# Kernel tuning notes

Hardware: AMD Instinct MI355X
Metric: run time of the kernel (lower is better)

The kernel has to match this reference:

```python
import collections
import functools
import itertools
import math
import jax
import jax.numpy as jnp
import numpy as np

# Weight space: RNN-like {W_ih:(784,512), W_hh:(512,512), b:(512,)}, channels last.
N0, N1, C_IN, C_OUT = 784, 512, 16, 16
PERM_SPEC = [[0, 1], [1, 1], [1]]  # perm-group label per dim of each leaf
N_TERMS = [11, 25, 9]  # equivariant basis terms per output leaf (Bell-number products)


def diagonal_slice(X, matching_dims):
    out = jnp.diagonal(X, axis1=matching_dims[0], axis2=matching_dims[1])
    for dim in matching_dims[2:]:
        out = jnp.diagonal(out, axis1=dim, axis2=-1)
    return out


def find_missing_indices(lstA, lstB):
    setB = set(lstB)
    return [i for i, el in enumerate(lstA) if el not in setB]


def get_repeated_idcs(lst):
    index_map = {}
    for index, item in enumerate(lst):
        index_map.setdefault(item, []).append(index)
    return [idcs for idcs in index_map.values() if len(idcs) > 1]


def match_dim_order(X, X_idcs, out_idcs):
    X_idcs_copy = X_idcs[:]
    perm = []
    for idx in out_idcs:
        if idx in X_idcs_copy:
            i = X_idcs_copy.index(idx)
            perm.append(i)
            X_idcs_copy[i] = None
    X = jnp.transpose(X, perm)
    return X, [X_idcs[i] for i in perm]


def remove_idcs(lst, idcs):
    return [l for i, l in enumerate(lst) if i not in idcs]


def move_dims_to_end(X, dims):
    new_in_order = remove_idcs(list(range(X.ndim)), dims) + dims
    return jnp.transpose(X, new_in_order)


def generate_partitions(items):
    if len(items) == 1:
        yield [items]
        return
    first = items[0]
    for subpart in generate_partitions(items[1:]):
        for n, subset in enumerate(subpart):
            yield subpart[:n] + [[first] + subset] + subpart[n + 1:]
        yield [[first]] + subpart


def valid_partitions(indices, perms):
    groups = collections.defaultdict(list)
    for index, perm in zip(indices, perms):
        groups[perm].append(index)
    parts_per_group = [list(generate_partitions(g)) for g in groups.values()]
    for p in itertools.product(*parts_per_group):
        yield [s for s in itertools.chain(*p)]


def gen_terms(out_spec, in_spec, out_shape, inp):
    """Basis terms of an equivariant linear map from in_spec to out_spec."""
    terms = []
    k1, k2 = len(out_spec), len(in_spec)
    for partition in valid_partitions(list(range(k1 + k2)), list(out_spec) + list(in_spec)):
        indices = [-1] * (k1 + k2)
        for subset_idx, subset in enumerate(partition):
            for dim in subset:
                indices[dim] = subset_idx
        out_indices, in_indices = indices[:k1], indices[k1:]
        term = inp
        # Collapse repeated input indices via diagonals.
        while (rep_idcs := get_repeated_idcs(in_indices)):
            term = diagonal_slice(term, rep_idcs[0])
            idx = in_indices[rep_idcs[0][0]]
            in_indices = remove_idcs(in_indices, rep_idcs[0])
            in_indices.append(idx)
        # Mean-reduce input dims that do not appear in the output.
        agg_idcs = find_missing_indices(in_indices, out_indices)
        term = jnp.mean(term, axis=agg_idcs)
        in_indices = remove_idcs(in_indices, agg_idcs)
        # Scatter onto diagonals for repeated output indices.
        for diag_set in get_repeated_idcs(out_indices):
            dim_size, out_idx = out_shape[diag_set[0]], out_indices[diag_set[0]]
            matching_in_dims = [i for i, idx in enumerate(in_indices) if idx == out_idx]
            num_new_dims = len(diag_set) - len(matching_in_dims)
            term = move_dims_to_end(term, matching_in_dims)
            new_term = jnp.zeros(term.shape + (dim_size,) * num_new_dims, dtype=term.dtype)
            diag_slice = (jnp.s_[:],) * (new_term.ndim - len(diag_set)) + (jnp.arange(dim_size),) * len(diag_set)
            if not matching_in_dims:
                term = jnp.expand_dims(term, axis=-1)
            term = new_term.at[diag_slice].add(term)
            in_indices = remove_idcs(in_indices, matching_in_dims)
            in_indices.extend([out_idx] * len(diag_set))
        term, in_indices = match_dim_order(term, in_indices, out_indices)
        term = jnp.expand_dims(term, axis=find_missing_indices(out_indices, in_indices))
        terms.append(term)
    return terms


def setup_inputs() -> dict:
    key = jax.random.key(0)
    ks = jax.random.split(key, 6)
    inp = {
        "w_ih": jax.random.normal(ks[0], (N0, N1, C_IN), jnp.float32),
        "w_hh": jax.random.normal(ks[1], (N1, N1, C_IN), jnp.float32),
        "b": jax.random.normal(ks[2], (N1, C_IN), jnp.float32),
    }
    for i, n in enumerate(N_TERMS):
        scale = math.sqrt(2.0 / (C_IN * n))  # 'he' init, fan_in = c_in * n_terms
        inp[f"theta_{i}"] = scale * jax.random.normal(ks[3 + i], (n, C_IN, C_OUT), jnp.float32)
        inp[f"bias_{i}"] = jnp.zeros((C_OUT,), jnp.float32)
    return inp


def reference(w_ih, w_hh, b, theta_0, theta_1, theta_2, bias_0, bias_1, bias_2):
    flat_params = [w_ih, w_hh, b]
    thetas = [theta_0, theta_1, theta_2]
    biases = [bias_0, bias_1, bias_2]
    outs = []
    for i in range(3):
        terms_i = []
        for j in range(3):
            gen = jax.vmap(
                functools.partial(gen_terms, PERM_SPEC[i], PERM_SPEC[j], flat_params[i].shape),
                in_axes=-1, out_axes=-1)
            terms_i.extend(gen(flat_params[j]))
        out = biases[i]
        for k, term in enumerate(terms_i):
            out = out + term @ thetas[i][k]  # [..., c_in] @ [c_in, c_out]
        outs.append(out)
    return tuple(outs)
```

## Files before the change

kernel.cpp:

```cpp
#include <hip/hip_runtime.h>


#define N0 784
#define N1 512

typedef float v4f __attribute__((ext_vector_type(4)));
typedef float v2f __attribute__((ext_vector_type(2)));

__device__ __forceinline__ float4 f4add(float4 a, float4 b) {
  a.x += b.x; a.y += b.y; a.z += b.z; a.w += b.w; return a;
}
__device__ __forceinline__ void nt_store4(float* p, float4 v) {
  v4f x; x[0] = v.x; x[1] = v.y; x[2] = v.z; x[3] = v.w;
  __builtin_nontemporal_store(x, (v4f*)p);
}
__device__ __forceinline__ void nt_store2(float* p, float x0, float x1) {
  v2f x; x[0] = x0; x[1] = x1;
  __builtin_nontemporal_store(x, (v2f*)p);
}

__global__ __launch_bounds__(256)
void k_stage1(const float* __restrict__ wih, const float* __restrict__ whh,
              float* __restrict__ rm_ih, float* __restrict__ cm_ih,
              float* __restrict__ rm_hh, float* __restrict__ cm_hh,
              float* __restrict__ d_hh) {
  __shared__ float4 red[256];
  int t = threadIdx.x, blk = blockIdx.x;
  float4 acc = make_float4(0.f, 0.f, 0.f, 0.f);
  float scale;
  float* dst;
  if (blk < N0) {
    const float4* row = (const float4*)(wih + (size_t)blk * 8192);
    for (int j = t; j < 2048; j += 256) acc = f4add(acc, row[j]);
    scale = 1.f / 512.f; dst = rm_ih + blk * 16;
  } else if (blk < N0 + N1) {
    int b = blk - N0, q = t & 3, g = t >> 2;
    for (int a = g; a < N0; a += 64)
      acc = f4add(acc, *(const float4*)(wih + (size_t)a * 8192 + b * 16 + q * 4));
    scale = 1.f / 784.f; dst = cm_ih + b * 16;
  } else if (blk < N0 + 2 * N1) {
    int b = blk - N0 - N1;
    const float4* row = (const float4*)(whh + (size_t)b * 8192);
    for (int j = t; j < 2048; j += 256) acc = f4add(acc, row[j]);
    scale = 1.f / 512.f; dst = rm_hh + b * 16;
  } else {
    int b = blk - N0 - 2 * N1, q = t & 3, g = t >> 2;
    for (int a = g; a < N1; a += 64)
      acc = f4add(acc, *(const float4*)(whh + (size_t)a * 8192 + b * 16 + q * 4));
    scale = 1.f / 512.f; dst = cm_hh + b * 16;
    if (t < 4) ((float4*)(d_hh + b * 16))[t] = *(const float4*)(whh + (size_t)b * 8192 + b * 16 + t * 4);
  }
  red[t] = acc; __syncthreads();
  #pragma unroll
  for (int s = 128; s >= 4; s >>= 1) {
    if (t < s) red[t] = f4add(red[t], red[t + s]);
    __syncthreads();
  }
  if (t < 4) {
    float4 m = red[t];
    ((float4*)dst)[t] = make_float4(m.x * scale, m.y * scale, m.z * scale, m.w * scale);
  }
}

__global__ __launch_bounds__(256)
void k_small(const float* __restrict__ rm_ih, const float* __restrict__ d_hh,
             const float* __restrict__ rm_hh, const float* __restrict__ bvec,
             float* __restrict__ gv_g) {
  __shared__ float4 red[256];
  int t = threadIdx.x, q = t & 3, g = t >> 2;
  const float* src; int n; float scale;
  switch (blockIdx.x) {
    case 0: src = rm_ih; n = N0; scale = 1.f / 784.f; break;
    case 1: src = d_hh;  n = N1; scale = 1.f / 512.f; break;
    case 2: src = rm_hh; n = N1; scale = 1.f / 512.f; break;
    default: src = bvec; n = N1; scale = 1.f / 512.f; break;
  }
  float4 acc = make_float4(0.f, 0.f, 0.f, 0.f);
  for (int a = g; a < n; a += 64) acc = f4add(acc, ((const float4*)src)[a * 4 + q]);
  red[t] = acc; __syncthreads();
  #pragma unroll
  for (int s = 128; s >= 4; s >>= 1) {
    if (t < s) red[t] = f4add(red[t], red[t + s]);
    __syncthreads();
  }
  if (t < 4) {
    float4 m = red[t];
    float* dst = gv_g + blockIdx.x * 16 + t * 4;
    dst[0] = m.x * scale; dst[1] = m.y * scale; dst[2] = m.z * scale; dst[3] = m.w * scale;
  }
}

__global__ __launch_bounds__(256)
void k_vec(const float* __restrict__ rm_ih, const float* __restrict__ cm_ih,
           const float* __restrict__ rm_hh, const float* __restrict__ cm_hh,
           const float* __restrict__ d_hh, const float* __restrict__ bvec,
           const float* __restrict__ gv_g,
           const float* __restrict__ th0, const float* __restrict__ bias0,
           const float* __restrict__ th1, const float* __restrict__ bias1,
           const float* __restrict__ th2, const float* __restrict__ bias2,
           float* __restrict__ A0C, float* __restrict__ B0,
           float* __restrict__ A1C, float* __restrict__ B1,
           float* __restrict__ DD1, float* __restrict__ out2) {
  __shared__ float th[11520];
  __shared__ float gvs[64];
  int t = threadIdx.x;
  {
    float4* t4 = (float4*)th;
    const float4* s0 = (const float4*)th0;
    const float4* s1 = (const float4*)th1;
    const float4* s2 = (const float4*)th2;
    for (int j = t; j < 704; j += 256) t4[j] = s0[j];
    for (int j = t; j < 1600; j += 256) t4[704 + j] = s1[j];
    for (int j = t; j < 576; j += 256) t4[2304 + j] = s2[j];
    if (t < 64) gvs[t] = gv_g[t];
  }
  __syncthreads();
  int co = t & 15;
  float c0 = bias0[co], c1 = bias1[co], e1 = 0.f, s2v = bias2[co];
  #pragma unroll
  for (int j = 0; j < 16; j++) {
    int o = j * 16 + co;
    float g0v = gvs[j], dm = gvs[16 + j], gh = gvs[32 + j], mv = gvs[48 + j];
    c0  += g0v * th[768 + o]         + dm * th[1280 + o]        + gh * th[2048 + o]        + mv * th[2560 + o];
    c1  += g0v * th[2816 + 1024 + o] + dm * th[2816 + 2304 + o] + gh * th[2816 + 4864 + o] + mv * th[2816 + 6144 + o];
    e1  += g0v * th[2816 + 512 + o]  + dm * th[2816 + 1792 + o] + gh * th[2816 + 4096 + o] + mv * th[2816 + 5632 + o];
    s2v += g0v * th[9216 + 256 + o]  + dm * th[9216 + 768 + o]  + gh * th[9216 + 1536 + o] + mv * th[9216 + 2048 + o];
  }
  int idx = blockIdx.x * 256 + t;
  int i = idx >> 4;
  float a0 = c0;
  {
    const float4* r4 = (const float4*)(rm_ih + i * 16);
    #pragma unroll
    for (int kq = 0; kq < 4; kq++) {
      float4 r = r4[kq];
      float vr[4] = { r.x, r.y, r.z, r.w };
      #pragma unroll
      for (int e = 0; e < 4; e++) a0 += vr[e] * th[256 + (kq * 4 + e) * 16 + co];
    }
  }
  A0C[idx] = a0;
  if (i < N1) {
    float b0a = 0.f, a1 = c1, b1a = 0.f, dd = e1, o2 = s2v;
    const float4* c4 = (const float4*)(cm_ih + i * 16);
    const float4* d4 = (const float4*)(d_hh + i * 16);
    const float4* r4 = (const float4*)(rm_hh + i * 16);
    const float4* m4 = (const float4*)(cm_hh + i * 16);
    const float4* v4 = (const float4*)(bvec + i * 16);
    #pragma unroll
    for (int kq = 0; kq < 4; kq++) {
      float4 cq = c4[kq], dq = d4[kq], rq = r4[kq], mq = m4[kq], vq = v4[kq];
      float vc[4] = { cq.x, cq.y, cq.z, cq.w };
      float vd[4] = { dq.x, dq.y, dq.z, dq.w };
      float vr[4] = { rq.x, rq.y, rq.z, rq.w };
      float vm[4] = { mq.x, mq.y, mq.z, mq.w };
      float vb[4] = { vq.x, vq.y, vq.z, vq.w };
      #pragma unroll
      for (int e = 0; e < 4; e++) {
        int o = (kq * 4 + e) * 16 + co;
        float cmi = vc[e], d = vd[e], r = vr[e], cm = vm[e], v = vb[e];
        b0a += cmi * th[512 + o]         + d * th[1024 + o]        + r * th[1536 + o]        + cm * th[1792 + o]        + v * th[2304 + o];
        a1  += cmi * th[2816 + 768 + o]  + d * th[2816 + 2048 + o] + r * th[2816 + 4352 + o] + cm * th[2816 + 4608 + o] + v * th[2816 + 5888 + o];
        b1a += cmi * th[2816 + 256 + o]  + d * th[2816 + 1536 + o] + r * th[2816 + 3072 + o] + cm * th[2816 + 3840 + o] + v * th[2816 + 5376 + o];
        dd  += cmi * th[2816 + 0 + o]    + d * th[2816 + 1280 + o] + r * th[2816 + 2560 + o] + cm * th[2816 + 3584 + o] + v * th[2816 + 5120 + o];
        o2  += cmi * th[9216 + 0 + o]    + d * th[9216 + 512 + o]  + r * th[9216 + 1024 + o] + cm * th[9216 + 1280 + o] + v * th[9216 + 1792 + o];
      }
    }
    B0[idx] = b0a; A1C[idx] = a1; B1[idx] = b1a; DD1[idx] = dd; out2[idx] = o2;
  }
}

__global__ __launch_bounds__(256)
void k_out(const float* __restrict__ wih, const float* __restrict__ whh,
           const float* __restrict__ th0, const float* __restrict__ th1,
           const float* __restrict__ A0C, const float* __restrict__ B0,
           const float* __restrict__ A1C, const float* __restrict__ B1,
           const float* __restrict__ DD1,
           float* __restrict__ out0, float* __restrict__ out1) {
  if (blockIdx.x < 1024) {
    int tid = blockIdx.x * 256 + threadIdx.x;
    int q = tid & 3;
    int slot = tid >> 2;
    const int nslots = (1024 * 256) >> 2;
    float4 tq[16];
    #pragma unroll
    for (int k = 0; k < 16; k++) tq[k] = *(const float4*)(th0 + k * 16 + q * 4);
    for (int p = slot; p < N0 * N1; p += nslots) {
      const float4* row = (const float4*)(wih + (size_t)p * 16);
      float4 r0 = row[0], r1 = row[1], r2 = row[2], r3 = row[3];
      int a = p >> 9, bb = p & 511;
      float4 acc = *(const float4*)(A0C + a * 16 + q * 4);
      float4 b4 = *(const float4*)(B0 + bb * 16 + q * 4);
      acc.x += b4.x; acc.y += b4.y; acc.z += b4.z; acc.w += b4.w;
      float wv[16] = { r0.x, r0.y, r0.z, r0.w, r1.x, r1.y, r1.z, r1.w,
                       r2.x, r2.y, r2.z, r2.w, r3.x, r3.y, r3.z, r3.w };
      #pragma unroll
      for (int k = 0; k < 16; k++) {
        acc.x += wv[k] * tq[k].x; acc.y += wv[k] * tq[k].y;
        acc.z += wv[k] * tq[k].z; acc.w += wv[k] * tq[k].w;
      }
      nt_store4(out0 + (size_t)p * 16 + q * 4, acc);
    }
  } else {
    int tid = (blockIdx.x - 1024) * 256 + threadIdx.x;
    int q = tid & 7;
    int slot = tid >> 3;
    const int nslots = (1024 * 256) >> 3;
    float2 tA[16], tB[16];
    #pragma unroll
    for (int k = 0; k < 16; k++) {
      tA[k] = *(const float2*)(th1 + 13 * 256 + k * 16 + q * 2);
      tB[k] = *(const float2*)(th1 + 11 * 256 + k * 16 + q * 2);
    }
    for (int p = slot; p < N1 * N1; p += nslots) {
      int a = p >> 9, b = p & 511;
      const float4* ra = (const float4*)(whh + (size_t)p * 16);
      const float4* rt = (const float4*)(whh + (size_t)((b << 9) | a) * 16);
      float4 a0 = ra[0], a1v = ra[1], a2 = ra[2], a3 = ra[3];
      float4 t0 = rt[0], t1v = rt[1], t2 = rt[2], t3 = rt[3];
      float2 acc = *(const float2*)(A1C + a * 16 + q * 2);
      float2 bb = *(const float2*)(B1 + b * 16 + q * 2);
      acc.x += bb.x; acc.y += bb.y;
      if (a == b) {
        float2 dd = *(const float2*)(DD1 + a * 16 + q * 2);
        acc.x += dd.x; acc.y += dd.y;
      }
      float ya[16] = { a0.x, a0.y, a0.z, a0.w, a1v.x, a1v.y, a1v.z, a1v.w,
                       a2.x, a2.y, a2.z, a2.w, a3.x, a3.y, a3.z, a3.w };
      float yt[16] = { t0.x, t0.y, t0.z, t0.w, t1v.x, t1v.y, t1v.z, t1v.w,
                       t2.x, t2.y, t2.z, t2.w, t3.x, t3.y, t3.z, t3.w };
      #pragma unroll
      for (int k = 0; k < 16; k++) {
        acc.x += ya[k] * tA[k].x + yt[k] * tB[k].x;
        acc.y += ya[k] * tA[k].y + yt[k] * tB[k].y;
      }
      nt_store2(out1 + (size_t)p * 16 + q * 2, acc.x, acc.y);
    }
  }
}

extern "C" void kernel_launch(void* const* d_in, const int* in_sizes, int n_in,
                              void* d_out, int out_size, void* d_ws, size_t ws_size,
                              hipStream_t stream) {
  const float* w_ih = (const float*)d_in[0];
  const float* w_hh = (const float*)d_in[1];
  const float* bvec = (const float*)d_in[2];
  const float *th0, *bias0, *th1, *bias1, *th2, *bias2;
  if (n_in >= 9 && in_sizes[4] == 16) {
    th0 = (const float*)d_in[3]; bias0 = (const float*)d_in[4];
    th1 = (const float*)d_in[5]; bias1 = (const float*)d_in[6];
    th2 = (const float*)d_in[7]; bias2 = (const float*)d_in[8];
  } else {
    th0 = (const float*)d_in[3]; th1 = (const float*)d_in[4]; th2 = (const float*)d_in[5];
    bias0 = (const float*)d_in[6]; bias1 = (const float*)d_in[7]; bias2 = (const float*)d_in[8];
  }
  float* ws    = (float*)d_ws;
  float* rm_ih = ws;
  float* cm_ih = rm_ih + 12544;
  float* rm_hh = cm_ih + 8192;
  float* cm_hh = rm_hh + 8192;
  float* d_hh  = cm_hh + 8192;
  float* A0C   = d_hh + 8192;
  float* B0    = A0C + 12544;
  float* A1C   = B0 + 8192;
  float* B1    = A1C + 8192;
  float* DD1   = B1 + 8192;
  float* gv_g  = DD1 + 8192;
  float* out0 = (float*)d_out;
  float* out1 = out0 + (size_t)N0 * N1 * 16;
  float* out2 = out1 + (size_t)N1 * N1 * 16;

  hipLaunchKernelGGL(k_stage1, dim3(N0 + 3 * N1), dim3(256), 0, stream,
                     w_ih, w_hh, rm_ih, cm_ih, rm_hh, cm_hh, d_hh);
  hipLaunchKernelGGL(k_small, dim3(4), dim3(256), 0, stream,
                     rm_ih, d_hh, rm_hh, bvec, gv_g);
  hipLaunchKernelGGL(k_vec, dim3(49), dim3(256), 0, stream,
                     rm_ih, cm_ih, rm_hh, cm_hh, d_hh, bvec, gv_g,
                     th0, bias0, th1, bias1, th2, bias2,
                     A0C, B0, A1C, B1, DD1, out2);
  hipLaunchKernelGGL(k_out, dim3(2048), dim3(256), 0, stream,
                     w_ih, w_hh, th0, th1, A0C, B0, A1C, B1, DD1, out0, out1);
}
```

Before: 150.4 us.

## Fuse row and column means into one pass with partial sums; LDS theta in output kernel

Stage 1 now reads each weight row once, computing both the row mean and a per-block partial column sum over four rows. A new reduction kernel combines those partials into the column means and also takes over the small global-mean work. Before this, the column-mean blocks made a second strided pass over both weight tensors. The output kernel now holds theta slices in shared memory instead of registers, and the w_hh branch gets twice as many blocks. The cost is an extra partial-sum buffer in workspace, plus LDS reads inside the hot inner loop.

```diff
diff --git a/kernel.cpp b/kernel.cpp
--- a/kernel.cpp
+++ b/kernel.cpp
@@ -3,6 +3,9 @@
 
 #define N0 784
 #define N1 512
+#define RPB 4
+#define NB_IH (N0 / RPB)
+#define NB_HH (N1 / RPB)
 
 typedef float v4f __attribute__((ext_vector_type(4)));
 typedef float v2f __attribute__((ext_vector_type(2)));
@@ -21,72 +24,107 @@
 
 __global__ __launch_bounds__(256)
 void k_stage1(const float* __restrict__ wih, const float* __restrict__ whh,
-              float* __restrict__ rm_ih, float* __restrict__ cm_ih,
-              float* __restrict__ rm_hh, float* __restrict__ cm_hh,
-              float* __restrict__ d_hh) {
-  __shared__ float4 red[256];
+              float* __restrict__ rm_ih, float* __restrict__ rm_hh,
+              float* __restrict__ d_hh,
+              float* __restrict__ part_ih, float* __restrict__ part_hh) {
+  __shared__ float4 colacc[2048];
+  __shared__ float4 redAll[RPB][256];
   int t = threadIdx.x, blk = blockIdx.x;
-  float4 acc = make_float4(0.f, 0.f, 0.f, 0.f);
-  float scale;
-  float* dst;
-  if (blk < N0) {
-    const float4* row = (const float4*)(wih + (size_t)blk * 8192);
-    for (int j = t; j < 2048; j += 256) acc = f4add(acc, row[j]);
-    scale = 1.f / 512.f; dst = rm_ih + blk * 16;
-  } else if (blk < N0 + N1) {
-    int b = blk - N0, q = t & 3, g = t >> 2;
-    for (int a = g; a < N0; a += 64)
-      acc = f4add(acc, *(const float4*)(wih + (size_t)a * 8192 + b * 16 + q * 4));
-    scale = 1.f / 784.f; dst = cm_ih + b * 16;
-  } else if (blk < N0 + 2 * N1) {
-    int b = blk - N0 - N1;
-    const float4* row = (const float4*)(whh + (size_t)b * 8192);
-    for (int j = t; j < 2048; j += 256) acc = f4add(acc, row[j]);
-    scale = 1.f / 512.f; dst = rm_hh + b * 16;
+  bool hh = blk >= NB_IH;
+  const float* W = hh ? whh : wih;
+  float* rm      = hh ? rm_hh : rm_ih;
+  float* part    = hh ? part_hh : part_ih;
+  int pblk = hh ? blk - NB_IH : blk;
+  int r0 = pblk * RPB;
+
+  #pragma unroll
+  for (int jj = 0; jj < 8; jj++) colacc[t + jj * 256] = make_float4(0.f, 0.f, 0.f, 0.f);
+  #pragma unroll
+  for (int r = 0; r < RPB; r++) {
+    const float4* row = (const float4*)(W + (size_t)(r0 + r) * 8192);
+    float4 v[8];
+    #pragma unroll
+    for (int jj = 0; jj < 8; jj++) v[jj] = row[t + jj * 256];
+    float4 racc = make_float4(0.f, 0.f, 0.f, 0.f);
+    #pragma unroll
+    for (int jj = 0; jj < 8; jj++) {
+      colacc[t + jj * 256] = f4add(colacc[t + jj * 256], v[jj]);
+      racc = f4add(racc, v[jj]);
+    }
+    redAll[r][t] = racc;
+  }
+  __syncthreads();
+  #pragma unroll
+  for (int s = 128; s >= 4; s >>= 1) {
+    if (t < s) {
+      #pragma unroll
+      for (int r = 0; r < RPB; r++) redAll[r][t] = f4add(redAll[r][t], redAll[r][t + s]);
+    }
+    __syncthreads();
+  }
+  if (t < 16) {
+    int r = t >> 2, q = t & 3;
+    float4 m = redAll[r][q];
+    const float s = 1.f / 512.f;
+    ((float4*)(rm + (r0 + r) * 16))[q] = make_float4(m.x * s, m.y * s, m.z * s, m.w * s);
+  }
+  if (hh && t < 64) {
+    int r = t >> 4, ci = t & 15;
+    d_hh[(r0 + r) * 16 + ci] = whh[(size_t)(r0 + r) * 8192 + (r0 + r) * 16 + ci];
+  }
+  float4* p4 = (float4*)(part + (size_t)pblk * 8192);
+  #pragma unroll
+  for (int jj = 0; jj < 8; jj++) p4[t + jj * 256] = colacc[t + jj * 256];
+}
+
+__global__ __launch_bounds__(1024)
+void k_red(const float* __restrict__ part_ih, const float* __restrict__ part_hh,
+           const float* __restrict__ rm_ih, const float* __restrict__ rm_hh,
+           const float* __restrict__ d_hh, const float* __restrict__ bvec,
+           float* __restrict__ cm_ih, float* __restrict__ cm_hh,
+           float* __restrict__ gv_g) {
+  __shared__ float lds[1024];
+  __shared__ float4 red4[1024];
+  int t = threadIdx.x, blk = blockIdx.x;
+  if (blk < 64) {
+    bool hh = blk >= 32;
+    int j = hh ? blk - 32 : blk;
+    const float* part = hh ? part_hh : part_ih;
+    int nP = hh ? NB_HH : NB_IH;
+    float scale = hh ? (1.f / 512.f) : (1.f / 784.f);
+    float* cm = hh ? cm_hh : cm_ih;
+    int sub = t & 255, py = t >> 8;
+    int per = (nP + 3) >> 2;
+    int p0 = py * per;
+    int p1 = p0 + per; if (p1 > nP) p1 = nP;
+    float acc = 0.f;
+    for (int p = p0; p < p1; p++) acc += part[(size_t)p * 8192 + j * 256 + sub];
+    lds[t] = acc; __syncthreads();
+    if (py == 0)
+      cm[j * 256 + sub] = (lds[sub] + lds[256 + sub] + lds[512 + sub] + lds[768 + sub]) * scale;
   } else {
-    int b = blk - N0 - 2 * N1, q = t & 3, g = t >> 2;
-    for (int a = g; a < N1; a += 64)
-      acc = f4add(acc, *(const float4*)(whh + (size_t)a * 8192 + b * 16 + q * 4));
-    scale = 1.f / 512.f; dst = cm_hh + b * 16;
-    if (t < 4) ((float4*)(d_hh + b * 16))[t] = *(const float4*)(whh + (size_t)b * 8192 + b * 16 + t * 4);
-  }
-  red[t] = acc; __syncthreads();
-  #pragma unroll
-  for (int s = 128; s >= 4; s >>= 1) {
-    if (t < s) red[t] = f4add(red[t], red[t + s]);
-    __syncthreads();
-  }
-  if (t < 4) {
-    float4 m = red[t];
-    ((float4*)dst)[t] = make_float4(m.x * scale, m.y * scale, m.z * scale, m.w * scale);
-  }
-}
-
-__global__ __launch_bounds__(256)
-void k_small(const float* __restrict__ rm_ih, const float* __restrict__ d_hh,
-             const float* __restrict__ rm_hh, const float* __restrict__ bvec,
-             float* __restrict__ gv_g) {
-  __shared__ float4 red[256];
-  int t = threadIdx.x, q = t & 3, g = t >> 2;
-  const float* src; int n; float scale;
-  switch (blockIdx.x) {
-    case 0: src = rm_ih; n = N0; scale = 1.f / 784.f; break;
-    case 1: src = d_hh;  n = N1; scale = 1.f / 512.f; break;
-    case 2: src = rm_hh; n = N1; scale = 1.f / 512.f; break;
-    default: src = bvec; n = N1; scale = 1.f / 512.f; break;
-  }
-  float4 acc = make_float4(0.f, 0.f, 0.f, 0.f);
-  for (int a = g; a < n; a += 64) acc = f4add(acc, ((const float4*)src)[a * 4 + q]);
-  red[t] = acc; __syncthreads();
-  #pragma unroll
-  for (int s = 128; s >= 4; s >>= 1) {
-    if (t < s) red[t] = f4add(red[t], red[t + s]);
-    __syncthreads();
-  }
-  if (t < 4) {
-    float4 m = red[t];
-    float* dst = gv_g + blockIdx.x * 16 + t * 4;
-    dst[0] = m.x * scale; dst[1] = m.y * scale; dst[2] = m.z * scale; dst[3] = m.w * scale;
+    int which = blk - 64;
+    const float* src; int n; float scale;
+    switch (which) {
+      case 0:  src = rm_ih; n = N0; scale = 1.f / 784.f; break;
+      case 1:  src = d_hh;  n = N1; scale = 1.f / 512.f; break;
+      case 2:  src = rm_hh; n = N1; scale = 1.f / 512.f; break;
+      default: src = bvec;  n = N1; scale = 1.f / 512.f; break;
+    }
+    int q = t & 3, g = t >> 2;
+    float4 acc = make_float4(0.f, 0.f, 0.f, 0.f);
+    for (int a = g; a < n; a += 256) acc = f4add(acc, ((const float4*)src)[a * 4 + q]);
+    red4[t] = acc; __syncthreads();
+    #pragma unroll
+    for (int s = 512; s >= 4; s >>= 1) {
+      if (t < s) red4[t] = f4add(red4[t], red4[t + s]);
+      __syncthreads();
+    }
+    if (t < 4) {
+      float4 m = red4[t];
+      float* dst = gv_g + which * 16 + t * 4;
+      dst[0] = m.x * scale; dst[1] = m.y * scale; dst[2] = m.z * scale; dst[3] = m.w * scale;
+    }
   }
 }
 
@@ -177,14 +215,17 @@
            const float* __restrict__ A1C, const float* __restrict__ B1,
            const float* __restrict__ DD1,
            float* __restrict__ out0, float* __restrict__ out1) {
+  __shared__ float t0s[256];
+  __shared__ float tAs[256];
+  __shared__ float tBs[256];
+  int t = threadIdx.x;
   if (blockIdx.x < 1024) {
-    int tid = blockIdx.x * 256 + threadIdx.x;
+    t0s[t] = th0[t];
+    __syncthreads();
+    int tid = blockIdx.x * 256 + t;
     int q = tid & 3;
     int slot = tid >> 2;
     const int nslots = (1024 * 256) >> 2;
-    float4 tq[16];
-    #pragma unroll
-    for (int k = 0; k < 16; k++) tq[k] = *(const float4*)(th0 + k * 16 + q * 4);
     for (int p = slot; p < N0 * N1; p += nslots) {
       const float4* row = (const float4*)(wih + (size_t)p * 16);
       float4 r0 = row[0], r1 = row[1], r2 = row[2], r3 = row[3];
@@ -196,22 +237,20 @@
                        r2.x, r2.y, r2.z, r2.w, r3.x, r3.y, r3.z, r3.w };
       #pragma unroll
       for (int k = 0; k < 16; k++) {
-        acc.x += wv[k] * tq[k].x; acc.y += wv[k] * tq[k].y;
-        acc.z += wv[k] * tq[k].z; acc.w += wv[k] * tq[k].w;
+        float4 tq = *(const float4*)(t0s + k * 16 + q * 4);
+        acc.x += wv[k] * tq.x; acc.y += wv[k] * tq.y;
+        acc.z += wv[k] * tq.z; acc.w += wv[k] * tq.w;
       }
       nt_store4(out0 + (size_t)p * 16 + q * 4, acc);
     }
   } else {
-    int tid = (blockIdx.x - 1024) * 256 + threadIdx.x;
+    tAs[t] = th1[13 * 256 + t];
+    tBs[t] = th1[11 * 256 + t];
+    __syncthreads();
+    int tid = (blockIdx.x - 1024) * 256 + t;
     int q = tid & 7;
     int slot = tid >> 3;
-    const int nslots = (1024 * 256) >> 3;
-    float2 tA[16], tB[16];
-    #pragma unroll
-    for (int k = 0; k < 16; k++) {
-      tA[k] = *(const float2*)(th1 + 13 * 256 + k * 16 + q * 2);
-      tB[k] = *(const float2*)(th1 + 11 * 256 + k * 16 + q * 2);
-    }
+    const int nslots = (2048 * 256) >> 3;
     for (int p = slot; p < N1 * N1; p += nslots) {
       int a = p >> 9, b = p & 511;
       const float4* ra = (const float4*)(whh + (size_t)p * 16);
@@ -231,8 +270,10 @@
                        t2.x, t2.y, t2.z, t2.w, t3.x, t3.y, t3.z, t3.w };
       #pragma unroll
       for (int k = 0; k < 16; k++) {
-        acc.x += ya[k] * tA[k].x + yt[k] * tB[k].x;
-        acc.y += ya[k] * tA[k].y + yt[k] * tB[k].y;
+        float2 tA = *(const float2*)(tAs + k * 16 + q * 2);
+        float2 tB = *(const float2*)(tBs + k * 16 + q * 2);
+        acc.x += ya[k] * tA.x + yt[k] * tB.x;
+        acc.y += ya[k] * tA.y + yt[k] * tB.y;
       }
       nt_store2(out1 + (size_t)p * 16 + q * 2, acc.x, acc.y);
     }
@@ -254,30 +295,33 @@
     th0 = (const float*)d_in[3]; th1 = (const float*)d_in[4]; th2 = (const float*)d_in[5];
     bias0 = (const float*)d_in[6]; bias1 = (const float*)d_in[7]; bias2 = (const float*)d_in[8];
   }
-  float* ws    = (float*)d_ws;
-  float* rm_ih = ws;
-  float* cm_ih = rm_ih + 12544;
-  float* rm_hh = cm_ih + 8192;
-  float* cm_hh = rm_hh + 8192;
-  float* d_hh  = cm_hh + 8192;
-  float* A0C   = d_hh + 8192;
-  float* B0    = A0C + 12544;
-  float* A1C   = B0 + 8192;
-  float* B1    = A1C + 8192;
-  float* DD1   = B1 + 8192;
-  float* gv_g  = DD1 + 8192;
+  float* ws      = (float*)d_ws;
+  float* rm_ih   = ws;
+  float* rm_hh   = rm_ih + 12544;
+  float* d_hh    = rm_hh + 8192;
+  float* cm_ih   = d_hh + 8192;
+  float* cm_hh   = cm_ih + 8192;
+  float* A0C     = cm_hh + 8192;
+  float* B0      = A0C + 12544;
+  float* A1C     = B0 + 8192;
+  float* B1      = A1C + 8192;
+  float* DD1     = B1 + 8192;
+  float* gv_g    = DD1 + 8192;
+  float* part_ih = gv_g + 128;
+  float* part_hh = part_ih + (size_t)NB_IH * 8192;
   float* out0 = (float*)d_out;
   float* out1 = out0 + (size_t)N0 * N1 * 16;
   float* out2 = out1 + (size_t)N1 * N1 * 16;
 
-  hipLaunchKernelGGL(k_stage1, dim3(N0 + 3 * N1), dim3(256), 0, stream,
-                     w_ih, w_hh, rm_ih, cm_ih, rm_hh, cm_hh, d_hh);
-  hipLaunchKernelGGL(k_small, dim3(4), dim3(256), 0, stream,
-                     rm_ih, d_hh, rm_hh, bvec, gv_g);
+  hipLaunchKernelGGL(k_stage1, dim3(NB_IH + NB_HH), dim3(256), 0, stream,
+                     w_ih, w_hh, rm_ih, rm_hh, d_hh, part_ih, part_hh);
+  hipLaunchKernelGGL(k_red, dim3(68), dim3(1024), 0, stream,
+                     part_ih, part_hh, rm_ih, rm_hh, d_hh, bvec,
+                     cm_ih, cm_hh, gv_g);
   hipLaunchKernelGGL(k_vec, dim3(49), dim3(256), 0, stream,
                      rm_ih, cm_ih, rm_hh, cm_hh, d_hh, bvec, gv_g,
                      th0, bias0, th1, bias1, th2, bias2,
                      A0C, B0, A1C, B1, DD1, out2);
-  hipLaunchKernelGGL(k_out, dim3(2048), dim3(256), 0, stream,
+  hipLaunchKernelGGL(k_out, dim3(3072), dim3(256), 0, stream,
                      w_ih, w_hh, th0, th1, A0C, B0, A1C, B1, DD1, out0, out1);
 }
```

After: 147.9 us. No clear change (-1.6%).
